# Kernel optimization log

Measured on AMD Instinct MI355X. Metric: run time of the kernel, lower is better.

## Reference

```python
import jax, jax.numpy as jnp
import numpy as np

B, N, E, FIN, D, A = 64, 512, 2048, 300, 256, 64
NH = 4
EPS = 1e-5


def setup_inputs() -> dict:
    ks = jax.random.split(jax.random.key(0), 32)
    lengths = 256 + jax.random.randint(ks[0], (B,), 0, N - 256 + 1)
    L = lengths[:, None]
    r = jax.random.randint(ks[1], (B, E), 0, 1 << 30)
    c = jax.random.randint(ks[2], (B, E), 0, 1 << 30)
    edge_row = r % L                                   # src in [0, len)
    edge_col = (edge_row + 1 + c % (L - 1)) % L        # dst != src, in [0, len)
    w = lambda k, sh, fan: jax.random.normal(k, sh, jnp.float32) / np.float32(np.sqrt(fan))
    b = lambda k, sh: 0.01 * jax.random.normal(k, sh, jnp.float32)
    return dict(
        x=jax.random.normal(ks[3], (B, N, FIN), jnp.float32),
        edge_attr=jax.random.normal(ks[4], (B, E, A), jnp.float32),
        edge_row=edge_row, edge_col=edge_col, lengths=lengths,
        W1=w(ks[5], (D, FIN), FIN), W2=w(ks[6], (D, A), A),
        W3=w(ks[7], (D, 2 * D), 2 * D), b3=b(ks[8], (D,)), gcn_bias=b(ks[9], (D,)),
        bn1_g=jnp.ones((D,)), bn1_b=jnp.zeros((D,)),
        in_proj_w=w(ks[10], (3 * D, D), D), in_proj_b=b(ks[11], (3 * D,)),
        out_proj_w=w(ks[12], (D, D), D), out_proj_b=b(ks[13], (D,)),
        ln1_g=jnp.ones((D,)), ln1_b=jnp.zeros((D,)),
        lin1_w=w(ks[14], (4 * D, D), D), lin1_b=b(ks[15], (4 * D,)),
        lin2_w=w(ks[16], (D, 4 * D), 4 * D), lin2_b=b(ks[17], (D,)),
        ln2_g=jnp.ones((D,)), ln2_b=jnp.zeros((D,)),
        bn2_g=jnp.ones((D,)), bn2_b=jnp.zeros((D,)),
        lin_w=w(ks[18], (2, 2 * D), 2 * D), lin_b=b(ks[19], (2,)),
        bn3_g=jnp.ones((2,)), bn3_b=jnp.zeros((2,)),
    )


def _bn(x, g, bt, axes):
    m = jnp.mean(x, axes, keepdims=True)
    v = jnp.mean((x - m) ** 2, axes, keepdims=True)
    return (x - m) / jnp.sqrt(v + EPS) * g + bt


def _ln(x, g, bt):
    m = jnp.mean(x, -1, keepdims=True)
    v = jnp.mean((x - m) ** 2, -1, keepdims=True)
    return (x - m) / jnp.sqrt(v + EPS) * g + bt


def _forward(x, edge_attr, edge_row, edge_col, lengths,
             W1, W2, W3, b3, gcn_bias, bn1_g, bn1_b,
             in_proj_w, in_proj_b, out_proj_w, out_proj_b, ln1_g, ln1_b,
             lin1_w, lin1_b, lin2_w, lin2_b, ln2_g, ln2_b, bn2_g, bn2_b,
             lin_w, lin_b, bn3_g, bn3_b):
    BN_ = B * N
    off = (jnp.arange(B, dtype=edge_row.dtype) * N)[:, None]
    row = (edge_row + off).reshape(-1)
    col = (edge_col + off).reshape(-1)
    sl = jnp.arange(BN_, dtype=row.dtype)            # one self-loop per node
    row_all = jnp.concatenate([row, sl])
    col_all = jnp.concatenate([col, sl])
    xs = x.reshape(BN_, FIN) @ W1.T                  # [BN, D]
    ea = edge_attr.reshape(B * E, A) @ W2.T          # [BE, D]
    ea_all = jnp.concatenate([ea, jnp.ones((BN_, D), xs.dtype)], 0)
    deg = jax.ops.segment_sum(jnp.ones_like(col_all, dtype=xs.dtype), col_all, BN_)
    dinv = deg ** -0.5                               # deg >= 1 (self loops)
    norm = dinv[row_all] * dinv[col_all]
    msg = norm[:, None] * (jnp.concatenate([xs[row_all], ea_all], -1) @ W3.T + b3)
    agg = jax.ops.segment_sum(msg, col_all, BN_) / deg[:, None]   # aggr='mean'
    h = jnp.tanh(agg + gcn_bias).reshape(B, N, D)
    mask = jnp.arange(N)[None, :] < lengths[:, None]              # pad_sequence zeros
    h = h * mask[..., None]
    h = _bn(h, bn1_g, bn1_b, (0, 1))
    # TransformerEncoderLayer (post-norm, relu, no dropout, no attn mask)
    qkv = h @ in_proj_w.T + in_proj_b
    q, k, v = jnp.split(qkv, 3, -1)
    dh = D // NH
    q = q.reshape(B, N, NH, dh); k = k.reshape(B, N, NH, dh); v = v.reshape(B, N, NH, dh)
    sc = jnp.einsum('bqhd,bkhd->bhqk', q, k) / np.float32(np.sqrt(dh))
    attn = jnp.einsum('bhqk,bkhd->bqhd', jax.nn.softmax(sc, -1), v).reshape(B, N, D)
    attn = attn @ out_proj_w.T + out_proj_b
    h1 = _ln(h + attn, ln1_g, ln1_b)
    ff = jax.nn.relu(h1 @ lin1_w.T + lin1_b) @ lin2_w.T + lin2_b
    h2 = _ln(h1 + ff, ln2_g, ln2_b)
    enc = _bn(h2, bn2_g, bn2_b, (0, 1))
    lenf = lengths.astype(enc.dtype)
    avg = jnp.sum(enc, 1) / lenf[:, None]            # sum over full padded length
    mx = jnp.max(jnp.where(mask[..., None], enc, -jnp.inf), 1)  # ragged max
    pool = jnp.concatenate([mx, avg], 1)
    res = _bn(pool @ lin_w.T + lin_b, bn3_g, bn3_b, (0,))
    return jax.nn.softmax(res, 1)


def reference(x, edge_attr, edge_row, edge_col, lengths,
              W1, W2, W3, b3, gcn_bias, bn1_g, bn1_b,
              in_proj_w, in_proj_b, out_proj_w, out_proj_b, ln1_g, ln1_b,
              lin1_w, lin1_b, lin2_w, lin2_b, ln2_g, ln2_b, bn2_g, bn2_b,
              lin_w, lin_b, bn3_g, bn3_b):
    return _forward(x, edge_attr, edge_row, edge_col, lengths,
                    W1, W2, W3, b3, gcn_bias, bn1_g, bn1_b,
                    in_proj_w, in_proj_b, out_proj_w, out_proj_b, ln1_g, ln1_b,
                    lin1_w, lin1_b, lin2_w, lin2_b, ln2_g, ln2_b, bn2_g, bn2_b,
                    lin_w, lin_b, bn3_g, bn3_b)
```

## Files before the change

### kernel.cpp

```cpp
#include <hip/hip_runtime.h>
#include <hip/hip_bf16.h>

#define BB   64
#define NN   512
#define EE   2048
#define FINK 300
#define DD   256
#define BN_TOT (BB*NN)
#define BE_TOT (BB*EE)
#define EPSF 1e-5f

using bf16 = __hip_bfloat16;
typedef unsigned short u16;
typedef __attribute__((ext_vector_type(8))) short short8;
typedef __attribute__((ext_vector_type(4))) float f32x4;
typedef __attribute__((ext_vector_type(4))) unsigned short u16x4;

__device__ __forceinline__ float tf(float x) { return x; }
__device__ __forceinline__ float tf(bf16 x)  { return __bfloat162float(x); }
__device__ __forceinline__ void  stv(float* p, float v) { *p = v; }
__device__ __forceinline__ void  stv(bf16*  p, float v) { *p = __float2bfloat16(v); }

__device__ __forceinline__ u16 f2bu(float f) {
    bf16 b = __float2bfloat16(f);
    return *(u16*)&b;
}
__device__ __forceinline__ void st4b(u16* p, f32x4 v)
{
    u16x4 o;
    o[0] = f2bu(v[0]); o[1] = f2bu(v[1]); o[2] = f2bu(v[2]); o[3] = f2bu(v[3]);
    *(u16x4*)p = o;
}

__device__ __forceinline__ void gload16(const void* g, void* l)
{
    __builtin_amdgcn_global_load_lds((const __attribute__((address_space(1))) void*)g,
                                     (__attribute__((address_space(3))) void*)l, 16, 0, 0);
}

__global__ void detect_kernel(const int* __restrict__ lengths, int* __restrict__ flags,
                              int* __restrict__ lenc)
{
    int wide = (lengths[1] == 0) ? 1 : 0;
    if (threadIdx.x == 0) flags[1] = wide;
    if (threadIdx.x < BB) lenc[threadIdx.x] = lengths[wide ? (threadIdx.x << 1) : threadIdx.x];
}

__global__ void conv_i2(const void* __restrict__ src1, int* __restrict__ dst1,
                        const void* __restrict__ src2, int* __restrict__ dst2,
                        int n, const int* __restrict__ flags)
{
    int i = blockIdx.x * 256 + threadIdx.x;
    int wide = flags[1];
    if (i < n) {
        dst1[i] = ((const int*)src1)[wide ? (i << 1) : i];
    } else if (i < 2 * n) {
        int k = i - n;
        dst2[k] = ((const int*)src2)[wide ? (k << 1) : k];
    }
}

__global__ void conv_pad(const float* __restrict__ src, u16* __restrict__ dst, int rows,
                         int sk, int dk)
{
    int dk4 = dk >> 2;
    int i = blockIdx.x * 256 + threadIdx.x;
    if (i >= rows * dk4) return;
    int r = i / dk4, c4 = (i - r * dk4) * 4;
    if (c4 < sk) {
        f32x4 v = *(const f32x4*)&src[(size_t)r * sk + c4];
        st4b(&dst[(size_t)r * dk + c4], v);
    } else {
        *(u16x4*)&dst[(size_t)r * dk + c4] = (u16x4){0, 0, 0, 0};
    }
}

__global__ void conv_w4(const float* __restrict__ s0, u16* __restrict__ d0,
                        const float* __restrict__ s1, u16* __restrict__ d1,
                        const float* __restrict__ s2, u16* __restrict__ d2,
                        const float* __restrict__ s3, u16* __restrict__ d3)
{
    int i = blockIdx.x * 256 + threadIdx.x;
    const float* s; u16* d; int off;
    if (i < 49152)       { s = s0; d = d0; off = i; }
    else if (i < 65536)  { s = s1; d = d1; off = i - 49152; }
    else if (i < 131072) { s = s2; d = d2; off = i - 65536; }
    else                 { s = s3; d = d3; off = i - 131072; }
    f32x4 v = *(const f32x4*)&s[(size_t)off * 4];
    st4b(&d[(size_t)off * 4], v);
}

__global__ void prep_W13(const float* __restrict__ W3, const float* __restrict__ W1,
                         u16* __restrict__ W13b)
{
    int d = blockIdx.x;
    int f = threadIdx.x;
    float s = 0.f;
    if (f < FINK) {
        for (int j = 0; j < 256; j++)
            s += W3[d * 512 + j] * W1[j * FINK + f];
    }
    W13b[d * 320 + f] = f2bu(s);
}

template<typename TC, int RELU>
__global__ __launch_bounds__(256)
void gemm_bf(const u16* __restrict__ A, const u16* __restrict__ W,
             const float* __restrict__ bias, TC* __restrict__ C,
             int M, int N, int K, int lda, int ldw)
{
    __shared__ u16 As[128 * 64];
    __shared__ u16 Ws[128 * 64];

    const int m0 = blockIdx.y * 128;
    const int n0 = blockIdx.x * 128;
    const int tid  = threadIdx.x;
    const int lane = tid & 63;
    const int wv   = tid >> 6;
    const int fr   = lane & 15;
    const int q8   = (lane >> 4) * 8;
    const int mb   = (wv >> 1) * 64;
    const int nb   = (wv & 1) * 64;

    const int r8  = lane >> 3;
    const int csw = 8 * ((lane & 7) ^ r8);
    const int frx = (fr & 7) << 3;

    f32x4 acc[4][4];
#pragma unroll
    for (int i = 0; i < 4; i++)
#pragma unroll
        for (int j = 0; j < 4; j++) acc[i][j] = (f32x4){0.f, 0.f, 0.f, 0.f};

    for (int k0 = 0; k0 < K; k0 += 64) {
        __syncthreads();
#pragma unroll
        for (int j = 0; j < 4; j++) {
            int rowA = m0 + wv * 32 + j * 8 + r8;
            int rowW = n0 + wv * 32 + j * 8 + r8;
            gload16(A + (size_t)rowA * lda + k0 + csw, &As[(wv * 32 + j * 8) * 64]);
            gload16(W + (size_t)rowW * ldw + k0 + csw, &Ws[(wv * 32 + j * 8) * 64]);
        }
        __syncthreads();

#pragma unroll
        for (int ks = 0; ks < 2; ks++) {
            int rc = (ks * 32 + q8) ^ frx;
            short8 af[4], bf[4];
#pragma unroll
            for (int i = 0; i < 4; i++) af[i] = *(const short8*)&As[(mb + i * 16 + fr) * 64 + rc];
#pragma unroll
            for (int j = 0; j < 4; j++) bf[j] = *(const short8*)&Ws[(nb + j * 16 + fr) * 64 + rc];
#pragma unroll
            for (int i = 0; i < 4; i++)
#pragma unroll
                for (int j = 0; j < 4; j++)
                    acc[i][j] = __builtin_amdgcn_mfma_f32_16x16x32_bf16(af[i], bf[j], acc[i][j], 0, 0, 0);
        }
    }

#pragma unroll
    for (int i = 0; i < 4; i++) {
#pragma unroll
        for (int j = 0; j < 4; j++) {
            int gn = n0 + nb + j * 16 + fr;
            float bv = bias ? bias[gn] : 0.f;
#pragma unroll
            for (int r = 0; r < 4; r++) {
                int gm = m0 + mb + i * 16 + (lane >> 4) * 4 + r;
                float v = acc[i][j][r] + bv;
                if (RELU) v = fmaxf(v, 0.f);
                stv(&C[(size_t)gm * N + gn], v);
            }
        }
    }
}

__global__ void prep_M(const float* __restrict__ W3, const float* __restrict__ W2,
                       u16* __restrict__ Mb, float* __restrict__ sb)
{
    int d = blockIdx.x, a = threadIdx.x;
    float s = 0.f;
    for (int j = 0; j < 256; j++)
        s += W3[d * 512 + 256 + j] * W2[j * 64 + a];
    Mb[d * 64 + a] = f2bu(s);
    if (a == 0) {
        float t = 0.f;
        for (int j = 0; j < 256; j++) t += W3[d * 512 + 256 + j];
        sb[d] = t;
    }
}

__global__ __launch_bounds__(512)
void sort_edges(const int* __restrict__ ecol, const int* __restrict__ erow,
                float* __restrict__ deg, int* __restrict__ node_off,
                uint2* __restrict__ edat)
{
    const int b = blockIdx.x;
    const int t = threadIdx.x;
    const int base = b * EE;
    __shared__ int cnt[512];
    __shared__ int tmp[512];
    __shared__ int off2[512];

    cnt[t] = 0;
    __syncthreads();
    for (int e = t; e < EE; e += 512) atomicAdd(&cnt[ecol[base + e]], 1);
    __syncthreads();

    int v = cnt[t];
    deg[b * NN + t] = (float)(v + 1);
    tmp[t] = v;
    __syncthreads();
    for (int s = 1; s < 512; s <<= 1) {
        int y = (t >= s) ? tmp[t - s] : 0;
        __syncthreads();
        tmp[t] += y;
        __syncthreads();
    }
    int excl = tmp[t] - v;
    node_off[b * NN + t] = excl;
    off2[t] = excl;
    __syncthreads();
    for (int e = t; e < EE; e += 512) {
        int c = ecol[base + e];
        int r = erow[base + e];
        int pos = atomicAdd(&off2[c], 1);
        float nrm = rsqrtf((float)((cnt[r] + 1) * (cnt[c] + 1)));
        edat[base + pos] = make_uint2(((unsigned)e << 16) | (unsigned)r,
                                      __float_as_uint(nrm));
    }
}

__global__ __launch_bounds__(256)
void edge_gather(const uint2* __restrict__ edat, const int* __restrict__ node_off,
                 const float* __restrict__ y1, const float* __restrict__ eattr,
                 float* __restrict__ agg1, u16* __restrict__ eaggb)
{
    const int j = blockIdx.x;
    const int b = j >> 9;
    const int cc = j & 511;
    const int tid  = threadIdx.x;
    const int wv   = tid >> 6;
    const int lane = tid & 63;
    const int start = node_off[j];
    const int end   = (cc == 511) ? EE : node_off[j + 1];

    f32x4 acc = (f32x4){0.f, 0.f, 0.f, 0.f};
    float acce = 0.f;
    for (int i = start + wv; i < end; i += 4) {
        uint2 ed = edat[(size_t)b * EE + i];
        float nw = __uint_as_float(ed.y);
        int r = (int)(ed.x & 0xffffu);
        int e = (int)(ed.x >> 16);
        f32x4 yv = *(const f32x4*)&y1[((size_t)(b * NN + r)) * 256 + lane * 4];
        acc += nw * yv;
        acce += nw * eattr[((size_t)(b * EE + e)) * 64 + lane];
    }

    __shared__ f32x4 redA[4][64];
    __shared__ float redB[4][64];
    redA[wv][lane] = acc;
    redB[wv][lane] = acce;
    __syncthreads();
    if (tid < 64) {
        f32x4 s = redA[0][tid];
        float se = redB[0][tid];
#pragma unroll
        for (int w = 1; w < 4; w++) { s += redA[w][tid]; se += redB[w][tid]; }
        *(f32x4*)&agg1[(size_t)j * 256 + tid * 4] = s;
        eaggb[(size_t)j * 64 + tid] = f2bu(se);
    }
}

__global__ __launch_bounds__(256)
void gcn_fin_stats(const float* __restrict__ agg1, float* __restrict__ aggM,
                   const float* __restrict__ y1, const float* __restrict__ sb,
                   const float* __restrict__ deg, const float* __restrict__ gcn_bias,
                   const int* __restrict__ lengths,
                   float* __restrict__ psum, float* __restrict__ psumsq)
{
    int wv = threadIdx.x >> 6, lane = threadIdx.x & 63;
    int d4 = lane * 4;
    f32x4 sv = *(const f32x4*)&sb[d4];
    f32x4 gb = *(const f32x4*)&gcn_bias[d4];
    f32x4 s = (f32x4){0.f, 0.f, 0.f, 0.f};
    f32x4 q = (f32x4){0.f, 0.f, 0.f, 0.f};
    for (int j = blockIdx.x * 4 + wv; j < BN_TOT; j += 2048) {
        size_t base = (size_t)j * 256 + d4;
        float inv = 1.f / deg[j];
        f32x4 a1 = *(const f32x4*)&agg1[base];
        f32x4 aM = *(const f32x4*)&aggM[base];
        f32x4 yv = *(const f32x4*)&y1[base];
        int b = j >> 9, pp = j & 511;
        bool live = (pp < lengths[b]);
        f32x4 o;
#pragma unroll
        for (int k = 0; k < 4; k++) {
            float a = (a1[k] + aM[k] + (yv[k] + sv[k]) * inv) * inv;
            o[k] = live ? tanhf(a + gb[k]) : 0.f;
        }
        *(f32x4*)&aggM[base] = o;
        s += o; q += o * o;
    }
    __shared__ f32x4 rs[4][64], rq[4][64];
    rs[wv][lane] = s; rq[wv][lane] = q;
    __syncthreads();
    if (threadIdx.x < 64) {
        f32x4 ts = rs[0][lane], tq = rq[0][lane];
#pragma unroll
        for (int w = 1; w < 4; w++) { ts += rs[w][lane]; tq += rq[w][lane]; }
        *(f32x4*)&psum[blockIdx.x * DD + lane * 4]   = ts;
        *(f32x4*)&psumsq[blockIdx.x * DD + lane * 4] = tq;
    }
}

__global__ void bn_reduce(const float* __restrict__ psum, const float* __restrict__ psumsq,
                          float* __restrict__ sums, float* __restrict__ sumsq)
{
    int arr = blockIdx.x & 1;
    int chunk = blockIdx.x >> 1;
    int d = threadIdx.x;
    const float* src = arr ? psumsq : psum;
    float acc = 0.f;
    int i0 = chunk * 32;
    for (int i = i0; i < i0 + 32; i++) acc += src[i * DD + d];
    atomicAdd(arr ? &sumsq[d] : &sums[d], acc);
}

__global__ void bn_apply(float* __restrict__ X, const float* __restrict__ sums,
                         const float* __restrict__ sumsq, const float* __restrict__ g,
                         const float* __restrict__ bt, int R, u16* __restrict__ dup)
{
    int idx4 = blockIdx.x * 256 + threadIdx.x;
    int d4 = (idx4 & 63) * 4;
    size_t base = (size_t)idx4 * 4;
    float invR = 1.f / (float)R;
    f32x4 sm = *(const f32x4*)&sums[d4];
    f32x4 sq = *(const f32x4*)&sumsq[d4];
    f32x4 gv = *(const f32x4*)&g[d4];
    f32x4 bv = *(const f32x4*)&bt[d4];
    f32x4 x  = *(const f32x4*)&X[base];
    f32x4 o;
#pragma unroll
    for (int k = 0; k < 4; k++) {
        float m   = sm[k] * invR;
        float var = sq[k] * invR - m * m;
        o[k] = (x[k] - m) * rsqrtf(fmaxf(var, 0.f) + EPSF) * gv[k] + bv[k];
    }
    *(f32x4*)&X[base] = o;
    if (dup) st4b(&dup[base], o);
}

__global__ __launch_bounds__(512, 2)
void attn_mfma(const bf16* __restrict__ qkv, u16* __restrict__ out)
{
    const int bid = blockIdx.x;
    const int qp = bid >> 8;
    const int pr = bid & 255;
    const int h  = pr & 3;
    const int b  = pr >> 2;

    const int tid  = threadIdx.x;
    const int lane = tid & 63;
    const int wv   = tid >> 6;
    const int fr   = lane & 15;
    const int quad = lane >> 4;
    const int q8   = quad * 8;

    __shared__ u16 Ks[128][72];
    __shared__ u16 Vts[64][136];
    __shared__ u16 Ps[128][68];

    const u16* qb = (const u16*)qkv;
    const size_t bb = (size_t)(b * NN);
    const float CE = 0.125f * 1.44269504f;

    short8 aq[2];
#pragma unroll
    for (int ks = 0; ks < 2; ks++)
        aq[ks] = *(const short8*)(qb + (bb + qp * 128 + wv * 16 + fr) * 768
                                  + h * 64 + ks * 32 + q8);

    f32x4 O[4];
    float m_i[4], l_i[4];
#pragma unroll
    for (int t = 0; t < 4; t++) {
        O[t] = (f32x4){0.f, 0.f, 0.f, 0.f};
        m_i[t] = -1e30f; l_i[t] = 0.f;
    }

    for (int c = 0; c < 4; c++) {
        __syncthreads();
#pragma unroll
        for (int i = 0; i < 2; i++) {
            int idx = i * 512 + tid;
            int r = idx >> 3, seg = idx & 7;
            uint4 u = *((const uint4*)(qb + (bb + c * 128 + r) * 768 + 256 + h * 64) + seg);
            *(uint4*)&Ks[r][seg * 8] = u;
            uint4 v = *((const uint4*)(qb + (bb + c * 128 + r) * 768 + 512 + h * 64) + seg);
            u16* dst = &Vts[seg * 8][r ^ (seg << 3)];
            dst[0*136] = (u16)(v.x & 0xffff); dst[1*136] = (u16)(v.x >> 16);
            dst[2*136] = (u16)(v.y & 0xffff); dst[3*136] = (u16)(v.y >> 16);
            dst[4*136] = (u16)(v.z & 0xffff); dst[5*136] = (u16)(v.z >> 16);
            dst[6*136] = (u16)(v.w & 0xffff); dst[7*136] = (u16)(v.w >> 16);
        }
        __syncthreads();

        f32x4 S[8];
#pragma unroll
        for (int t = 0; t < 8; t++) S[t] = (f32x4){0.f, 0.f, 0.f, 0.f};
        __builtin_amdgcn_s_setprio(1);
#pragma unroll
        for (int ks = 0; ks < 2; ks++) {
#pragma unroll
            for (int t = 0; t < 8; t++) {
                short8 bk = *(const short8*)&Ks[t * 16 + fr][ks * 32 + q8];
                S[t] = __builtin_amdgcn_mfma_f32_16x16x32_bf16(aq[ks], bk, S[t], 0, 0, 0);
            }
        }
        __builtin_amdgcn_s_setprio(0);

        float mc[4];
#pragma unroll
        for (int r = 0; r < 4; r++) {
            float mm = -1e30f;
#pragma unroll
            for (int t = 0; t < 8; t++) mm = fmaxf(mm, S[t][r]);
            mc[r] = mm;
        }
#pragma unroll
        for (int msk = 1; msk < 16; msk <<= 1)
#pragma unroll
            for (int r = 0; r < 4; r++) mc[r] = fmaxf(mc[r], __shfl_xor(mc[r], msk));

        float alpha[4], ls[4];
#pragma unroll
        for (int r = 0; r < 4; r++) {
            float mn = fmaxf(m_i[r], mc[r]);
            alpha[r] = __builtin_amdgcn_exp2f((m_i[r] - mn) * CE);
            m_i[r] = mn;
            ls[r] = 0.f;
        }
#pragma unroll
        for (int t = 0; t < 4; t++)
#pragma unroll
            for (int r = 0; r < 4; r++) O[t][r] *= alpha[r];

#pragma unroll
        for (int hf = 0; hf < 2; hf++) {
#pragma unroll
            for (int tl = 0; tl < 4; tl++) {
                int t = hf * 4 + tl;
#pragma unroll
                for (int r = 0; r < 4; r++) {
                    float p = __builtin_amdgcn_exp2f((S[t][r] - m_i[r]) * CE);
                    Ps[wv * 16 + quad * 4 + r][tl * 16 + fr] = f2bu(p);
                    ls[r] += p;
                }
            }
            __builtin_amdgcn_s_setprio(1);
#pragma unroll
            for (int ks = 0; ks < 2; ks++) {
                short8 ap = *(const short8*)&Ps[wv * 16 + fr][ks * 32 + q8];
                int g = hf * 2 + ks;
#pragma unroll
                for (int t = 0; t < 4; t++) {
                    short8 bv = *(const short8*)&Vts[t * 16 + fr]
                                    [(g * 32 + q8) ^ ((t * 2 + (fr >> 3)) << 3)];
                    O[t] = __builtin_amdgcn_mfma_f32_16x16x32_bf16(ap, bv, O[t], 0, 0, 0);
                }
            }
            __builtin_amdgcn_s_setprio(0);
        }

#pragma unroll
        for (int msk = 1; msk < 16; msk <<= 1)
#pragma unroll
            for (int r = 0; r < 4; r++) ls[r] += __shfl_xor(ls[r], msk);
#pragma unroll
        for (int r = 0; r < 4; r++) l_i[r] = l_i[r] * alpha[r] + ls[r];
    }

#pragma unroll
    for (int t = 0; t < 4; t++)
#pragma unroll
        for (int r = 0; r < 4; r++) {
            int q = qp * 128 + wv * 16 + quad * 4 + r;
            out[(bb + q) * 256 + h * 64 + t * 16 + fr] = f2bu(O[t][r] / l_i[r]);
        }
}

__global__ void add_ln_kernel(const float* __restrict__ X, const float* __restrict__ Y,
                              const float* __restrict__ g, const float* __restrict__ bt,
                              float* __restrict__ out, u16* __restrict__ dup)
{
    int wv = threadIdx.x >> 6, lane = threadIdx.x & 63;
    int row = blockIdx.x * 4 + wv;
    size_t base = (size_t)row * DD + lane * 4;
    f32x4 v = *(const f32x4*)&X[base] + *(const f32x4*)&Y[base];
    float s = v[0] + v[1] + v[2] + v[3];
#pragma unroll
    for (int m = 1; m < 64; m <<= 1) s += __shfl_xor(s, m);
    float mean = s * (1.f / DD);
    f32x4 d;
#pragma unroll
    for (int k = 0; k < 4; k++) d[k] = v[k] - mean;
    float q = d[0]*d[0] + d[1]*d[1] + d[2]*d[2] + d[3]*d[3];
#pragma unroll
    for (int m = 1; m < 64; m <<= 1) q += __shfl_xor(q, m);
    float inv = rsqrtf(q * (1.f / DD) + EPSF);
    f32x4 gv = *(const f32x4*)&g[lane * 4];
    f32x4 bv = *(const f32x4*)&bt[lane * 4];
    f32x4 o;
#pragma unroll
    for (int k = 0; k < 4; k++) o[k] = d[k] * inv * gv[k] + bv[k];
    *(f32x4*)&out[base] = o;
    if (dup) st4b(&dup[base], o);
}

__global__ __launch_bounds__(256)
void add_ln_stats(const float* __restrict__ X, const float* __restrict__ Y,
                  const float* __restrict__ g, const float* __restrict__ bt,
                  float* __restrict__ out,
                  float* __restrict__ psum, float* __restrict__ psumsq)
{
    int wv = threadIdx.x >> 6, lane = threadIdx.x & 63;
    f32x4 gv = *(const f32x4*)&g[lane * 4];
    f32x4 bv = *(const f32x4*)&bt[lane * 4];
    f32x4 s = (f32x4){0.f, 0.f, 0.f, 0.f};
    f32x4 qacc = (f32x4){0.f, 0.f, 0.f, 0.f};
    for (int row = blockIdx.x * 4 + wv; row < BN_TOT; row += 2048) {
        size_t base = (size_t)row * DD + lane * 4;
        f32x4 v = *(const f32x4*)&X[base] + *(const f32x4*)&Y[base];
        float sm = v[0] + v[1] + v[2] + v[3];
#pragma unroll
        for (int m = 1; m < 64; m <<= 1) sm += __shfl_xor(sm, m);
        float mean = sm * (1.f / DD);
        f32x4 d;
#pragma unroll
        for (int k = 0; k < 4; k++) d[k] = v[k] - mean;
        float qq = d[0]*d[0] + d[1]*d[1] + d[2]*d[2] + d[3]*d[3];
#pragma unroll
        for (int m = 1; m < 64; m <<= 1) qq += __shfl_xor(qq, m);
        float inv = rsqrtf(qq * (1.f / DD) + EPSF);
        f32x4 o;
#pragma unroll
        for (int k = 0; k < 4; k++) o[k] = d[k] * inv * gv[k] + bv[k];
        *(f32x4*)&out[base] = o;
        s += o; qacc += o * o;
    }
    __shared__ f32x4 rs[4][64], rq[4][64];
    rs[wv][lane] = s; rq[wv][lane] = qacc;
    __syncthreads();
    if (threadIdx.x < 64) {
        f32x4 ts = rs[0][lane], tq = rq[0][lane];
#pragma unroll
        for (int w = 1; w < 4; w++) { ts += rs[w][lane]; tq += rq[w][lane]; }
        *(f32x4*)&psum[blockIdx.x * DD + lane * 4]   = ts;
        *(f32x4*)&psumsq[blockIdx.x * DD + lane * 4] = tq;
    }
}

__global__ void pool_norm(const float* __restrict__ enc, const int* __restrict__ lengths,
                          const float* __restrict__ sums, const float* __restrict__ sumsq,
                          const float* __restrict__ g, const float* __restrict__ bt,
                          int R, float* __restrict__ poolbuf)
{
    int b = blockIdx.x;
    int wv = threadIdx.x >> 6, lane = threadIdx.x & 63;
    int L = lengths[b];
    if (L < 1) L = 1;
    float invR = 1.f / (float)R;
    f32x4 sm = *(const f32x4*)&sums[lane * 4];
    f32x4 sq = *(const f32x4*)&sumsq[lane * 4];
    f32x4 gv = *(const f32x4*)&g[lane * 4];
    f32x4 bv = *(const f32x4*)&bt[lane * 4];
    f32x4 mean, rsv;
#pragma unroll
    for (int k = 0; k < 4; k++) {
        mean[k] = sm[k] * invR;
        float var = sq[k] * invR - mean[k] * mean[k];
        rsv[k] = rsqrtf(fmaxf(var, 0.f) + EPSF) * gv[k];
    }
    f32x4 s  = (f32x4){0.f, 0.f, 0.f, 0.f};
    f32x4 mx = (f32x4){-1e30f, -1e30f, -1e30f, -1e30f};
    for (int n = wv; n < NN; n += 4) {
        f32x4 v = *(const f32x4*)&enc[((size_t)b * NN + n) * DD + lane * 4];
#pragma unroll
        for (int k = 0; k < 4; k++) v[k] = (v[k] - mean[k]) * rsv[k] + bv[k];
        s += v;
        if (n < L) {
#pragma unroll
            for (int k = 0; k < 4; k++) mx[k] = fmaxf(mx[k], v[k]);
        }
    }
    __shared__ f32x4 rs[4][64], rm[4][64];
    rs[wv][lane] = s; rm[wv][lane] = mx;
    __syncthreads();
    if (threadIdx.x < 64) {
        f32x4 ts = rs[0][lane], tm = rm[0][lane];
#pragma unroll
        for (int w = 1; w < 4; w++) {
            ts += rs[w][lane];
#pragma unroll
            for (int k = 0; k < 4; k++) tm[k] = fmaxf(tm[k], rm[w][lane][k]);
        }
        float invL = 1.f / (float)L;
#pragma unroll
        for (int k = 0; k < 4; k++) {
            poolbuf[b * 512 + lane * 4 + k]       = tm[k];
            poolbuf[b * 512 + 256 + lane * 4 + k] = ts[k] * invL;
        }
    }
}

__global__ void head_kernel(const float* __restrict__ poolbuf, const float* __restrict__ lin_w,
                            const float* __restrict__ lin_b, const float* __restrict__ g,
                            const float* __restrict__ bt, float* __restrict__ out)
{
    int b = threadIdx.x;
    float r0 = lin_b[0], r1 = lin_b[1];
    for (int k = 0; k < 512; k++) {
        float p = poolbuf[b * 512 + k];
        r0 += p * lin_w[k];
        r1 += p * lin_w[512 + k];
    }
    __shared__ float s0[64], s1[64], mstat[4];
    s0[b] = r0; s1[b] = r1; __syncthreads();
    if (b == 0) {
        float a0 = 0, a1 = 0, q0 = 0, q1 = 0;
        for (int i = 0; i < 64; i++) { a0 += s0[i]; a1 += s1[i]; }
        a0 *= (1.f / 64.f); a1 *= (1.f / 64.f);
        for (int i = 0; i < 64; i++) {
            float d0 = s0[i] - a0, d1 = s1[i] - a1;
            q0 += d0 * d0; q1 += d1 * d1;
        }
        mstat[0] = a0; mstat[1] = a1; mstat[2] = q0 * (1.f / 64.f); mstat[3] = q1 * (1.f / 64.f);
    }
    __syncthreads();
    float z0 = (r0 - mstat[0]) * rsqrtf(mstat[2] + EPSF) * g[0] + bt[0];
    float z1 = (r1 - mstat[1]) * rsqrtf(mstat[3] + EPSF) * g[1] + bt[1];
    float mx = fmaxf(z0, z1);
    float e0 = __expf(z0 - mx), e1 = __expf(z1 - mx);
    float inv = 1.f / (e0 + e1);
    out[b * 2 + 0] = e0 * inv;
    out[b * 2 + 1] = e1 * inv;
}

extern "C" void kernel_launch(void* const* d_in, const int* in_sizes, int n_in,
                              void* d_out, int out_size, void* d_ws, size_t ws_size,
                              hipStream_t stream)
{
    (void)in_sizes; (void)n_in; (void)out_size; (void)ws_size;
    const float* x          = (const float*)d_in[0];
    const float* edge_attr  = (const float*)d_in[1];
    const float* W1         = (const float*)d_in[5];
    const float* W2         = (const float*)d_in[6];
    const float* W3         = (const float*)d_in[7];
    const float* b3         = (const float*)d_in[8];
    const float* gcn_bias   = (const float*)d_in[9];
    const float* bn1_g      = (const float*)d_in[10];
    const float* bn1_b      = (const float*)d_in[11];
    const float* in_proj_w  = (const float*)d_in[12];
    const float* in_proj_b  = (const float*)d_in[13];
    const float* out_proj_w = (const float*)d_in[14];
    const float* out_proj_b = (const float*)d_in[15];
    const float* ln1_g      = (const float*)d_in[16];
    const float* ln1_b      = (const float*)d_in[17];
    const float* lin1_w     = (const float*)d_in[18];
    const float* lin1_b     = (const float*)d_in[19];
    const float* lin2_w     = (const float*)d_in[20];
    const float* lin2_b     = (const float*)d_in[21];
    const float* ln2_g      = (const float*)d_in[22];
    const float* ln2_b      = (const float*)d_in[23];
    const float* bn2_g      = (const float*)d_in[24];
    const float* bn2_b      = (const float*)d_in[25];
    const float* lin_w      = (const float*)d_in[26];
    const float* lin_b      = (const float*)d_in[27];
    const float* bn3_g      = (const float*)d_in[28];
    const float* bn3_b      = (const float*)d_in[29];

    char* p = (char*)d_ws;
    u16*   big   = (u16*)p;   p += (size_t)BN_TOT * 1024 * 2;
    float* bufA  = (float*)p; p += (size_t)BN_TOT * 256 * 4;
    float* bufB  = (float*)p; p += (size_t)BN_TOT * 256 * 4;
    float* bufC  = (float*)p; p += (size_t)BN_TOT * 256 * 4;
    u16*   bufP  = (u16*)p;   p += (size_t)BN_TOT * 256 * 2;
    float* deg   = (float*)p; p += (size_t)BN_TOT * 4;
    u16*   Mb    = (u16*)p;   p += 256 * 64 * 2;
    float* sb    = (float*)p; p += 1024;
    float* stats = (float*)p; p += 4 * 256 * 4;
    float* psum  = (float*)p; p += 512 * 256 * 4;
    float* psumsq= (float*)p; p += 512 * 256 * 4;
    float* poolbuf=(float*)p; p += 64 * 512 * 4;
    int*   flags = (int*)p;   p += 256;
    int*   erc   = (int*)p;   p += BE_TOT * 4;
    int*   ecc   = (int*)p;   p += BE_TOT * 4;
    int*   lenc  = (int*)p;   p += 256;
    uint2* edat  = (uint2*)p; p += (size_t)BE_TOT * 8;
    int*   noff  = (int*)p;   p += BN_TOT * 4;
    u16*   W13b  = (u16*)p;   p += 256 * 320 * 2;
    u16*   ipwb  = (u16*)p;   p += 768 * 256 * 2;
    u16*   opwb  = (u16*)p;   p += 256 * 256 * 2;
    u16*   l1wb  = (u16*)p;   p += 1024 * 256 * 2;
    u16*   l2wb  = (u16*)p;   p += 256 * 1024 * 2;

    u16* xb    = big;
    u16* eaggb = big + (size_t)BN_TOT * (320+256);
    bf16* qkv  = (bf16*)big;
    bf16* ffa  = (bf16*)big;

    float* y1      = bufB;
    float* agg1    = bufC;
    float* aggM    = bufA;
    float* h       = bufA;
    u16*   hb      = bufP;
    u16*   attnoutb= bufP;
    float* attnp   = bufB;
    float* h1      = bufC;
    u16*   h1b     = bufP;
    float* ffb     = bufA;
    float* h2      = bufB;

    hipMemsetAsync(stats, 0, 4 * 256 * 4, stream);

    detect_kernel<<<1, 64, 0, stream>>>((const int*)d_in[4], flags, lenc);
    conv_i2<<<(2 * BE_TOT + 255) / 256, 256, 0, stream>>>(d_in[2], erc, d_in[3], ecc,
                                                          BE_TOT, flags);

    conv_pad<<<(BN_TOT * 80 + 255) / 256, 256, 0, stream>>>(x, xb, BN_TOT, FINK, 320);
    conv_w4<<<768, 256, 0, stream>>>(in_proj_w, ipwb, out_proj_w, opwb,
                                     lin1_w, l1wb, lin2_w, l2wb);

    prep_W13<<<256, 320, 0, stream>>>(W3, W1, W13b);
    prep_M<<<256, 64, 0, stream>>>(W3, W2, Mb, sb);
    sort_edges<<<BB, 512, 0, stream>>>(ecc, erc, deg, noff, edat);

    gemm_bf<float, 0><<<dim3(2, 256), 256, 0, stream>>>(
        xb, W13b, b3, y1, BN_TOT, 256, 320, 320, 320);

    edge_gather<<<BN_TOT, 256, 0, stream>>>(edat, noff, y1, edge_attr, agg1, eaggb);
    gemm_bf<float, 0><<<dim3(2, 256), 256, 0, stream>>>(
        eaggb, Mb, nullptr, aggM, BN_TOT, 256, 64, 64, 64);

    gcn_fin_stats<<<512, 256, 0, stream>>>(agg1, aggM, y1, sb, deg, gcn_bias, lenc,
                                           psum, psumsq);
    bn_reduce<<<32, 256, 0, stream>>>(psum, psumsq, stats, stats + 256);
    bn_apply<<<BN_TOT / 4, 256, 0, stream>>>(h, stats, stats + 256, bn1_g, bn1_b, BN_TOT, hb);

    gemm_bf<bf16, 0><<<dim3(6, 256), 256, 0, stream>>>(
        hb, ipwb, in_proj_b, qkv, BN_TOT, 768, 256, 256, 256);

    attn_mfma<<<BB * 4 * 4, 512, 0, stream>>>(qkv, attnoutb);

    gemm_bf<float, 0><<<dim3(2, 256), 256, 0, stream>>>(
        attnoutb, opwb, out_proj_b, attnp, BN_TOT, 256, 256, 256, 256);

    add_ln_kernel<<<BN_TOT / 4, 256, 0, stream>>>(h, attnp, ln1_g, ln1_b, h1, h1b);

    gemm_bf<bf16, 1><<<dim3(8, 256), 256, 0, stream>>>(
        h1b, l1wb, lin1_b, ffa, BN_TOT, 1024, 256, 256, 256);
    gemm_bf<float, 0><<<dim3(2, 256), 256, 0, stream>>>(
        (const u16*)ffa, l2wb, lin2_b, ffb, BN_TOT, 256, 1024, 1024, 1024);

    add_ln_stats<<<512, 256, 0, stream>>>(h1, ffb, ln2_g, ln2_b, h2, psum, psumsq);
    bn_reduce<<<32, 256, 0, stream>>>(psum, psumsq, stats + 512, stats + 768);

    pool_norm<<<64, 256, 0, stream>>>(h2, lenc, stats + 512, stats + 768,
                                      bn2_g, bn2_b, BN_TOT, poolbuf);
    head_kernel<<<1, 64, 0, stream>>>(poolbuf, lin_w, lin_b, bn3_g, bn3_b, (float*)d_out);
}
```

Before: 557.6 us.

## Fuse GCN finalize and BN stats into edge-attr GEMM epilogue; remap gather blocks

Replaces the separate edge-attribute GEMM and the gcn_fin_stats kernel with one GEMM (K=64) whose epilogue adds agg1 and the self-loop term, applies tanh with the length mask, writes H and accumulates per-column sum and sum-of-squares through LDS atomics into per-block partials. This removes the write and re-read of the intermediate aggM buffer and one kernel launch. The epilogue loads agg1 and y1 in the MFMA output layout, which is less coalesced than the old vectorised pass. Separately, edge_gather blocks are remapped so consecutive block IDs stride across eight node chunks, presumably to keep each batch's y1 rows local to one XCD's cache.

```diff
diff --git a/kernel.cpp b/kernel.cpp
--- a/kernel.cpp
+++ b/kernel.cpp
@@ -176,6 +176,101 @@
     }
 }
 
+__global__ __launch_bounds__(256)
+void gemm_gcn(const u16* __restrict__ A, const u16* __restrict__ W,
+              const float* __restrict__ agg1, const float* __restrict__ y1,
+              const float* __restrict__ sb, const float* __restrict__ deg,
+              const float* __restrict__ gcn_bias, const int* __restrict__ lengths,
+              float* __restrict__ H, float* __restrict__ psum, float* __restrict__ psumsq)
+{
+    __shared__ u16 As[128 * 64];
+    __shared__ u16 Ws[128 * 64];
+    __shared__ float colsum[128], colsq[128];
+
+    const int m0 = blockIdx.y * 128;
+    const int n0 = blockIdx.x * 128;
+    const int bid = blockIdx.y * 2 + blockIdx.x;
+    const int tid  = threadIdx.x;
+    const int lane = tid & 63;
+    const int wv   = tid >> 6;
+    const int fr   = lane & 15;
+    const int quad = lane >> 4;
+    const int q8   = quad * 8;
+    const int mb   = (wv >> 1) * 64;
+    const int nb   = (wv & 1) * 64;
+
+    const int r8  = lane >> 3;
+    const int csw = 8 * ((lane & 7) ^ r8);
+    const int frx = (fr & 7) << 3;
+
+    if (tid < 128) { colsum[tid] = 0.f; colsq[tid] = 0.f; }
+
+#pragma unroll
+    for (int j = 0; j < 4; j++) {
+        int rowA = m0 + wv * 32 + j * 8 + r8;
+        int rowW = n0 + wv * 32 + j * 8 + r8;
+        gload16(A + (size_t)rowA * 64 + csw, &As[(wv * 32 + j * 8) * 64]);
+        gload16(W + (size_t)rowW * 64 + csw, &Ws[(wv * 32 + j * 8) * 64]);
+    }
+    __syncthreads();
+
+    f32x4 acc[4][4];
+#pragma unroll
+    for (int i = 0; i < 4; i++)
+#pragma unroll
+        for (int j = 0; j < 4; j++) acc[i][j] = (f32x4){0.f, 0.f, 0.f, 0.f};
+
+#pragma unroll
+    for (int ks = 0; ks < 2; ks++) {
+        int rc = (ks * 32 + q8) ^ frx;
+        short8 af[4], bf[4];
+#pragma unroll
+        for (int i = 0; i < 4; i++) af[i] = *(const short8*)&As[(mb + i * 16 + fr) * 64 + rc];
+#pragma unroll
+        for (int j = 0; j < 4; j++) bf[j] = *(const short8*)&Ws[(nb + j * 16 + fr) * 64 + rc];
+#pragma unroll
+        for (int i = 0; i < 4; i++)
+#pragma unroll
+            for (int j = 0; j < 4; j++)
+                acc[i][j] = __builtin_amdgcn_mfma_f32_16x16x32_bf16(af[i], bf[j], acc[i][j], 0, 0, 0);
+    }
+
+    float lsum[4] = {0.f, 0.f, 0.f, 0.f};
+    float lsq[4]  = {0.f, 0.f, 0.f, 0.f};
+#pragma unroll
+    for (int i = 0; i < 4; i++) {
+#pragma unroll
+        for (int r = 0; r < 4; r++) {
+            int gm = m0 + mb + i * 16 + quad * 4 + r;
+            float inv = 1.f / deg[gm];
+            int bb = gm >> 9, pp = gm & 511;
+            bool live = (pp < lengths[bb]);
+#pragma unroll
+            for (int j = 0; j < 4; j++) {
+                int gn = n0 + nb + j * 16 + fr;
+                size_t idx = (size_t)gm * 256 + gn;
+                float a = (acc[i][j][r] + agg1[idx] + (y1[idx] + sb[gn]) * inv) * inv;
+                float o = live ? tanhf(a + gcn_bias[gn]) : 0.f;
+                H[idx] = o;
+                lsum[j] += o; lsq[j] += o * o;
+            }
+        }
+    }
+#pragma unroll
+    for (int j = 0; j < 4; j++) {
+        int lc = nb + j * 16 + fr;
+        atomicAdd(&colsum[lc], lsum[j]);
+        atomicAdd(&colsq[lc],  lsq[j]);
+    }
+    __syncthreads();
+    if (tid < 128) {
+        psum  [(size_t)bid * 256 + n0 + tid] = colsum[tid];
+        psumsq[(size_t)bid * 256 + n0 + tid] = colsq[tid];
+        psum  [(size_t)bid * 256 + (n0 ^ 128) + tid] = 0.f;
+        psumsq[(size_t)bid * 256 + (n0 ^ 128) + tid] = 0.f;
+    }
+}
+
 __global__ void prep_M(const float* __restrict__ W3, const float* __restrict__ W2,
                        u16* __restrict__ Mb, float* __restrict__ sb)
 {
@@ -237,7 +332,8 @@
                  const float* __restrict__ y1, const float* __restrict__ eattr,
                  float* __restrict__ agg1, u16* __restrict__ eaggb)
 {
-    const int j = blockIdx.x;
+    const int bi = blockIdx.x;
+    const int j = (bi & 7) * 4096 + (bi >> 3);
     const int b = j >> 9;
     const int cc = j & 511;
     const int tid  = threadIdx.x;
@@ -270,48 +366,6 @@
         for (int w = 1; w < 4; w++) { s += redA[w][tid]; se += redB[w][tid]; }
         *(f32x4*)&agg1[(size_t)j * 256 + tid * 4] = s;
         eaggb[(size_t)j * 64 + tid] = f2bu(se);
-    }
-}
-
-__global__ __launch_bounds__(256)
-void gcn_fin_stats(const float* __restrict__ agg1, float* __restrict__ aggM,
-                   const float* __restrict__ y1, const float* __restrict__ sb,
-                   const float* __restrict__ deg, const float* __restrict__ gcn_bias,
-                   const int* __restrict__ lengths,
-                   float* __restrict__ psum, float* __restrict__ psumsq)
-{
-    int wv = threadIdx.x >> 6, lane = threadIdx.x & 63;
-    int d4 = lane * 4;
-    f32x4 sv = *(const f32x4*)&sb[d4];
-    f32x4 gb = *(const f32x4*)&gcn_bias[d4];
-    f32x4 s = (f32x4){0.f, 0.f, 0.f, 0.f};
-    f32x4 q = (f32x4){0.f, 0.f, 0.f, 0.f};
-    for (int j = blockIdx.x * 4 + wv; j < BN_TOT; j += 2048) {
-        size_t base = (size_t)j * 256 + d4;
-        float inv = 1.f / deg[j];
-        f32x4 a1 = *(const f32x4*)&agg1[base];
-        f32x4 aM = *(const f32x4*)&aggM[base];
-        f32x4 yv = *(const f32x4*)&y1[base];
-        int b = j >> 9, pp = j & 511;
-        bool live = (pp < lengths[b]);
-        f32x4 o;
-#pragma unroll
-        for (int k = 0; k < 4; k++) {
-            float a = (a1[k] + aM[k] + (yv[k] + sv[k]) * inv) * inv;
-            o[k] = live ? tanhf(a + gb[k]) : 0.f;
-        }
-        *(f32x4*)&aggM[base] = o;
-        s += o; q += o * o;
-    }
-    __shared__ f32x4 rs[4][64], rq[4][64];
-    rs[wv][lane] = s; rq[wv][lane] = q;
-    __syncthreads();
-    if (threadIdx.x < 64) {
-        f32x4 ts = rs[0][lane], tq = rq[0][lane];
-#pragma unroll
-        for (int w = 1; w < 4; w++) { ts += rs[w][lane]; tq += rq[w][lane]; }
-        *(f32x4*)&psum[blockIdx.x * DD + lane * 4]   = ts;
-        *(f32x4*)&psumsq[blockIdx.x * DD + lane * 4] = tq;
     }
 }
 
@@ -713,7 +767,6 @@
 
     float* y1      = bufB;
     float* agg1    = bufC;
-    float* aggM    = bufA;
     float* h       = bufA;
     u16*   hb      = bufP;
     u16*   attnoutb= bufP;
@@ -741,11 +794,9 @@
         xb, W13b, b3, y1, BN_TOT, 256, 320, 320, 320);
 
     edge_gather<<<BN_TOT, 256, 0, stream>>>(edat, noff, y1, edge_attr, agg1, eaggb);
-    gemm_bf<float, 0><<<dim3(2, 256), 256, 0, stream>>>(
-        eaggb, Mb, nullptr, aggM, BN_TOT, 256, 64, 64, 64);
-
-    gcn_fin_stats<<<512, 256, 0, stream>>>(agg1, aggM, y1, sb, deg, gcn_bias, lenc,
-                                           psum, psumsq);
+
+    gemm_gcn<<<dim3(2, 256), 256, 0, stream>>>(
+        eaggb, Mb, agg1, y1, sb, deg, gcn_bias, lenc, h, psum, psumsq);
     bn_reduce<<<32, 256, 0, stream>>>(psum, psumsq, stats, stats + 256);
     bn_apply<<<BN_TOT / 4, 256, 0, stream>>>(h, stats, stats + 256, bn1_g, bn1_b, BN_TOT, hb);
 
```

New measurement: 582.6 us. 1.04x slower.
